# Performance work log

Hardware: AMD Instinct MI355X
Metric: run time of the kernel (lower is better)

## Reference

```python
import jax, jax.numpy as jnp
import numpy as np

N_PART = 22      # alanine dipeptide atoms
N_DIM = 3
H_IN = 8         # h_initial feature dim (before time concat)
HID = 64
N_LAYERS = 4
BATCH = 1024
E_LOCAL = N_PART * (N_PART - 1)  # fully connected, both directions


def _make_edges(batch):
    rows, cols = [], []
    for i in range(N_PART):
        for j in range(i + 1, N_PART):
            rows += [i, j]; cols += [j, i]
    rows = np.asarray(rows, np.int32); cols = np.asarray(cols, np.int32)
    offs = (np.arange(batch, dtype=np.int32) * N_PART)[:, None]
    return (jnp.asarray((rows[None, :] + offs).reshape(-1)),
            jnp.asarray((cols[None, :] + offs).reshape(-1)))


def setup_inputs() -> dict:
    key = jax.random.key(0)
    ks = jax.random.split(key, 16)
    g = lambda k, shape, s=0.1: jax.random.normal(k, shape, jnp.float32) * s
    rows, cols = _make_edges(BATCH)
    return {
        "t": jax.random.uniform(ks[0], (BATCH, 1), jnp.float32),
        "xs": jax.random.normal(ks[1], (BATCH, N_PART * N_DIM), jnp.float32),
        "h_initial": g(ks[2], (N_PART, H_IN), 1.0),
        "emb_w": g(ks[3], (H_IN + 1, HID)), "emb_b": jnp.zeros((HID,), jnp.float32),
        "edge_w1": g(ks[4], (N_LAYERS, 2 * HID + 2, HID)), "edge_b1": jnp.zeros((N_LAYERS, HID), jnp.float32),
        "edge_w2": g(ks[5], (N_LAYERS, HID, HID)), "edge_b2": jnp.zeros((N_LAYERS, HID), jnp.float32),
        "node_w1": g(ks[6], (N_LAYERS, 2 * HID, HID)), "node_b1": jnp.zeros((N_LAYERS, HID), jnp.float32),
        "node_w2": g(ks[7], (N_LAYERS, HID, HID)), "node_b2": jnp.zeros((N_LAYERS, HID), jnp.float32),
        "coord_w1": g(ks[8], (N_LAYERS, HID, HID)), "coord_b1": jnp.zeros((N_LAYERS, HID), jnp.float32),
        "coord_w2": g(ks[9], (N_LAYERS, HID, 1)),
        "rows": rows, "cols": cols,
    }


def reference(t, xs, h_initial, emb_w, emb_b,
              edge_w1, edge_b1, edge_w2, edge_b2,
              node_w1, node_b1, node_w2, node_b2,
              coord_w1, coord_b1, coord_w2, rows, cols):
    B = xs.shape[0]
    NN = B * N_PART
    x0 = xs.reshape(NN, N_DIM)
    # node features: tiled h_initial + time channel
    h = jnp.tile(h_initial[None], (B, 1, 1)).reshape(NN, H_IN)
    tt = jnp.tile(t, (1, N_PART)).reshape(NN, 1)
    h = jnp.concatenate([h, tt], axis=-1)                       # [NN, H_IN+1]
    # static edge attribute: initial squared distances
    edge_attr = jnp.sum((x0[rows] - x0[cols]) ** 2, axis=1, keepdims=True)  # [E,1]

    h = h @ emb_w + emb_b                                       # embedding (no act)
    x = x0
    for l in range(N_LAYERS):
        diff = x[rows] - x[cols]                                # [E,3]
        radial = jnp.sum(diff ** 2, axis=1, keepdims=True)      # [E,1]
        diff = diff / (jnp.sqrt(radial) + 1.0)                  # norm_diff=True
        # edge model
        e_in = jnp.concatenate([h[rows], h[cols], radial, edge_attr], axis=1)
        m = jax.nn.silu(e_in @ edge_w1[l] + edge_b1[l])
        m = jax.nn.silu(m @ edge_w2[l] + edge_b2[l])            # [E,HID]
        # coord model (coord_mlp last layer has no bias; coords_weight=1, agg='sum')
        phi_x = jax.nn.silu(m @ coord_w1[l] + coord_b1[l]) @ coord_w2[l]  # [E,1]
        x = x + jax.ops.segment_sum(diff * phi_x, rows, num_segments=NN)
        # node model (recurrent residual)
        agg = jax.ops.segment_sum(m, rows, num_segments=NN)     # [NN,HID]
        n_in = jnp.concatenate([h, agg], axis=1)
        h = h + (jax.nn.silu(n_in @ node_w1[l] + node_b1[l]) @ node_w2[l] + node_b2[l])

    vel = (x - x0).reshape(B, N_PART, N_DIM)
    vel = vel - jnp.mean(vel, axis=1, keepdims=True)            # remove_mean
    return vel.reshape(B, N_PART * N_DIM)
```

## Files before the change

### kernel.cpp

```cpp
#include <hip/hip_runtime.h>


#define NPART   22
#define NDIM    3
#define XDIM    (NPART * NDIM)
#define H_IN    8
#define HID     64
#define NLAYERS 4
#define EPB     (NPART * (NPART - 1))
#define BLOCK   256

__device__ __forceinline__ float silu_f(float x) {
    return __fdividef(x, 1.0f + __expf(-x));
}

#define ACC16(ARR, WPTR, E0) do {                                   \
    const float4* _w4 = (const float4*)(WPTR);                      \
    _Pragma("unroll")                                               \
    for (int _q = 0; _q < 16; ++_q) {                               \
        float4 _w = _w4[_q];                                        \
        ARR[4*_q+0] = fmaf((E0), _w.x, ARR[4*_q+0]);                \
        ARR[4*_q+1] = fmaf((E0), _w.y, ARR[4*_q+1]);                \
        ARR[4*_q+2] = fmaf((E0), _w.z, ARR[4*_q+2]);                \
        ARR[4*_q+3] = fmaf((E0), _w.w, ARR[4*_q+3]);                \
    }                                                               \
} while (0)

#define ACC8(ARR, WPTR, E0) do {                                    \
    const float4* _w4 = (const float4*)(WPTR);                      \
    float4 _wa = _w4[0], _wb = _w4[1];                              \
    ARR[0] = fmaf((E0), _wa.x, ARR[0]);                             \
    ARR[1] = fmaf((E0), _wa.y, ARR[1]);                             \
    ARR[2] = fmaf((E0), _wa.z, ARR[2]);                             \
    ARR[3] = fmaf((E0), _wa.w, ARR[3]);                             \
    ARR[4] = fmaf((E0), _wb.x, ARR[4]);                             \
    ARR[5] = fmaf((E0), _wb.y, ARR[5]);                             \
    ARR[6] = fmaf((E0), _wb.z, ARR[6]);                             \
    ARR[7] = fmaf((E0), _wb.w, ARR[7]);                             \
} while (0)

__global__ void __launch_bounds__(BLOCK)
w2_transpose_kernel(const float* __restrict__ w2, float* __restrict__ w2t) {
    int l = blockIdx.x;
    for (int i = threadIdx.x; i < HID * HID; i += BLOCK) {
        int k = i >> 6, j = i & 63;
        w2t[l * HID * HID + j * HID + k] = w2[l * HID * HID + k * HID + j];
    }
}

__device__ __forceinline__ void edge_rc(int e, int& r, int& c) {
    int k = e / NPART;
    r = e - k * NPART;
    c = r + 1 + k;
    if (c >= NPART) c -= NPART;
}

#define WC_RW   0
#define WC_EA   64
#define WC_EB2  128
#define WC_CB1  192
#define WC_CW2  256
#define WC_N    320

template <bool TRANSPOSED>
__global__ void __launch_bounds__(BLOCK)
egnn_fused_kernel(const float* __restrict__ t_in,
                  const float* __restrict__ xs,
                  const float* __restrict__ h_init,
                  const float* __restrict__ emb_w,
                  const float* __restrict__ emb_b,
                  const float* __restrict__ edge_w1,
                  const float* __restrict__ edge_b1,
                  const float* __restrict__ edge_w2x,
                  const float* __restrict__ edge_b2,
                  const float* __restrict__ node_w1,
                  const float* __restrict__ node_b1,
                  const float* __restrict__ node_w2,
                  const float* __restrict__ node_b2,
                  const float* __restrict__ coord_w1,
                  const float* __restrict__ coord_b1,
                  const float* __restrict__ coord_w2,
                  float*       __restrict__ out) {
    __shared__ float h_s   [HID * NPART];
    __shared__ float hagg_s[HID * NPART];
    __shared__ float ns_s  [HID * NPART];
    __shared__ float pr_s  [HID * NPART];
    __shared__ float pc_s  [HID * NPART];
    __shared__ float wc_s  [WC_N];
    __shared__ float x_s[XDIM], x0_s[XDIM], xacc_s[XDIM];
    __shared__ float ea_s[EPB];
    __shared__ float mean_s[NDIM];

    const int b   = blockIdx.x;
    const int tid = threadIdx.x;
    const float tval = t_in[b];

    if (tid < XDIM) {
        float v = xs[b * XDIM + tid];
        x0_s[tid] = v;
        x_s[tid]  = v;
    }
    for (int idx = tid; idx < NPART * HID; idx += BLOCK) {
        int n = idx >> 6, j = idx & 63;
        float acc = emb_b[j] + tval * emb_w[H_IN * HID + j];
#pragma unroll
        for (int k = 0; k < H_IN; ++k)
            acc = fmaf(h_init[n * H_IN + k], emb_w[k * HID + j], acc);
        h_s[j * NPART + n] = acc;
    }
    __syncthreads();
    for (int e = tid; e < EPB; e += BLOCK) {
        int r, c; edge_rc(e, r, c);
        float dx = x0_s[r*3+0] - x0_s[c*3+0];
        float dy = x0_s[r*3+1] - x0_s[c*3+1];
        float dz = x0_s[r*3+2] - x0_s[c*3+2];
        ea_s[e] = dx*dx + dy*dy + dz*dz;
    }
    __syncthreads();

#pragma unroll 1
    for (int l = 0; l < NLAYERS; ++l) {
        const float* ew1 = edge_w1  + l * (2*HID + 2) * HID;
        const float* eb1 = edge_b1  + l * HID;
        const float* w2x = edge_w2x + l * HID * HID;
        const float* eb2 = edge_b2  + l * HID;
        const float* cw1 = coord_w1 + l * HID * HID;
        const float* cb1 = coord_b1 + l * HID;
        const float* cw2 = coord_w2 + l * HID;
        const float* nw1 = node_w1  + l * 2 * HID * HID;
        const float* nb1 = node_b1  + l * HID;
        const float* nw2 = node_w2  + l * HID * HID;
        const float* nb2 = node_b2  + l * HID;

        for (int idx = tid; idx < NPART * HID; idx += BLOCK) hagg_s[idx] = 0.0f;
        if (tid < XDIM) xacc_s[tid] = 0.0f;
        for (int idx = tid; idx < WC_N; idx += BLOCK) {
            int g = idx >> 6, j = idx & 63;
            float v;
            if      (g == 0) v = ew1[(2 * HID) * HID + j];
            else if (g == 1) v = ew1[(2 * HID + 1) * HID + j];
            else if (g == 2) v = eb2[j];
            else if (g == 3) v = cb1[j];
            else             v = cw2[j];
            wc_s[idx] = v;
        }

        if (tid < NPART * 8) {
            int n = tid >> 3, jg = tid & 7;
            float pr[8], pc[8];
            {
                const float4* b4 = (const float4*)(eb1 + jg * 8);
                float4 wa = b4[0], wb = b4[1];
                pr[0]=wa.x; pr[1]=wa.y; pr[2]=wa.z; pr[3]=wa.w;
                pr[4]=wb.x; pr[5]=wb.y; pr[6]=wb.z; pr[7]=wb.w;
            }
#pragma unroll
            for (int jj = 0; jj < 8; ++jj) pc[jj] = 0.0f;
#pragma unroll 1
            for (int k = 0; k < HID; ++k) {
                float e0 = h_s[k * NPART + n];
                ACC8(pr, ew1 + k * HID + jg * 8, e0);
                ACC8(pc, ew1 + (HID + k) * HID + jg * 8, e0);
            }
#pragma unroll
            for (int jj = 0; jj < 8; ++jj) {
                pr_s[(jg * 8 + jj) * NPART + n] = pr[jj];
                pc_s[(jg * 8 + jj) * NPART + n] = pc[jj];
            }
        }
        __syncthreads();

#pragma unroll 1
        for (int e = tid; e < EPB; e += BLOCK) {
            int r, c; edge_rc(e, r, c);
            float dx = x_s[r*3+0] - x_s[c*3+0];
            float dy = x_s[r*3+1] - x_s[c*3+1];
            float dz = x_s[r*3+2] - x_s[c*3+2];
            float radial = dx*dx + dy*dy + dz*dz;
            float invn = __fdividef(1.0f, sqrtf(radial) + 1.0f);
            float ux = dx * invn, uy = dy * invn, uz = dz * invn;
            float ea = ea_s[e];

            float a[HID];
#pragma unroll
            for (int j = 0; j < HID; ++j) {
                float v = pr_s[j * NPART + r] + pc_s[j * NPART + c];
                v = fmaf(radial, wc_s[WC_RW + j], v);
                v = fmaf(ea,     wc_s[WC_EA + j], v);
                a[j] = silu_f(v);
            }

            float t1[HID];
#pragma unroll
            for (int q = 0; q < 16; ++q) {
                float4 w = ((const float4*)(wc_s + WC_CB1))[q];
                t1[4*q+0] = w.x; t1[4*q+1] = w.y;
                t1[4*q+2] = w.z; t1[4*q+3] = w.w;
            }

#pragma unroll 2
            for (int j = 0; j < HID; ++j) {
                float m0, m1, m2, m3;
                if constexpr (TRANSPOSED) {
                    const float4* w4 = (const float4*)(w2x + j * HID);
                    m0 = wc_s[WC_EB2 + j]; m1 = 0.0f; m2 = 0.0f; m3 = 0.0f;
#pragma unroll
                    for (int q = 0; q < 4; ++q) {
                        float4 wA = w4[4*q+0], wB = w4[4*q+1];
                        float4 wC = w4[4*q+2], wD = w4[4*q+3];
                        m0 = fmaf(a[16*q+ 0], wA.x, m0);
                        m0 = fmaf(a[16*q+ 1], wA.y, m0);
                        m0 = fmaf(a[16*q+ 2], wA.z, m0);
                        m0 = fmaf(a[16*q+ 3], wA.w, m0);
                        m1 = fmaf(a[16*q+ 4], wB.x, m1);
                        m1 = fmaf(a[16*q+ 5], wB.y, m1);
                        m1 = fmaf(a[16*q+ 6], wB.z, m1);
                        m1 = fmaf(a[16*q+ 7], wB.w, m1);
                        m2 = fmaf(a[16*q+ 8], wC.x, m2);
                        m2 = fmaf(a[16*q+ 9], wC.y, m2);
                        m2 = fmaf(a[16*q+10], wC.z, m2);
                        m2 = fmaf(a[16*q+11], wC.w, m2);
                        m3 = fmaf(a[16*q+12], wD.x, m3);
                        m3 = fmaf(a[16*q+13], wD.y, m3);
                        m3 = fmaf(a[16*q+14], wD.z, m3);
                        m3 = fmaf(a[16*q+15], wD.w, m3);
                    }
                } else {
                    m0 = wc_s[WC_EB2 + j]; m1 = 0.0f; m2 = 0.0f; m3 = 0.0f;
#pragma unroll
                    for (int k = 0; k < HID; k += 4) {
                        m0 = fmaf(a[k+0], w2x[(k+0) * HID + j], m0);
                        m1 = fmaf(a[k+1], w2x[(k+1) * HID + j], m1);
                        m2 = fmaf(a[k+2], w2x[(k+2) * HID + j], m2);
                        m3 = fmaf(a[k+3], w2x[(k+3) * HID + j], m3);
                    }
                }
                float mj = silu_f((m0 + m1) + (m2 + m3));
                atomicAdd(&hagg_s[j * NPART + r], mj);
                ACC16(t1, cw1 + j * HID, mj);
            }

            float phi = 0.0f;
#pragma unroll
            for (int q = 0; q < 16; ++q) {
                float4 w = ((const float4*)(wc_s + WC_CW2))[q];
                phi = fmaf(silu_f(t1[4*q+0]), w.x, phi);
                phi = fmaf(silu_f(t1[4*q+1]), w.y, phi);
                phi = fmaf(silu_f(t1[4*q+2]), w.z, phi);
                phi = fmaf(silu_f(t1[4*q+3]), w.w, phi);
            }
            atomicAdd(&xacc_s[r*3+0], ux * phi);
            atomicAdd(&xacc_s[r*3+1], uy * phi);
            atomicAdd(&xacc_s[r*3+2], uz * phi);
        }
        __syncthreads();

        if (tid < NPART * 8) {
            int n = tid >> 3, jg = tid & 7;
            float acc[8];
            {
                const float4* b4 = (const float4*)(nb1 + jg * 8);
                float4 wa = b4[0], wb = b4[1];
                acc[0]=wa.x; acc[1]=wa.y; acc[2]=wa.z; acc[3]=wa.w;
                acc[4]=wb.x; acc[5]=wb.y; acc[6]=wb.z; acc[7]=wb.w;
            }
#pragma unroll 1
            for (int k = 0; k < HID; ++k) {
                float e0 = h_s[k * NPART + n];
                ACC8(acc, nw1 + k * HID + jg * 8, e0);
            }
#pragma unroll 1
            for (int k = 0; k < HID; ++k) {
                float e0 = hagg_s[k * NPART + n];
                ACC8(acc, nw1 + (HID + k) * HID + jg * 8, e0);
            }
#pragma unroll
            for (int jj = 0; jj < 8; ++jj)
                ns_s[(jg * 8 + jj) * NPART + n] = silu_f(acc[jj]);
        }
        __syncthreads();
        if (tid < NPART * 8) {
            int n = tid >> 3, jg = tid & 7;
            float acc[8];
            {
                const float4* b4 = (const float4*)(nb2 + jg * 8);
                float4 wa = b4[0], wb = b4[1];
                acc[0]=wa.x; acc[1]=wa.y; acc[2]=wa.z; acc[3]=wa.w;
                acc[4]=wb.x; acc[5]=wb.y; acc[6]=wb.z; acc[7]=wb.w;
            }
#pragma unroll 1
            for (int k = 0; k < HID; ++k) {
                float e0 = ns_s[k * NPART + n];
                ACC8(acc, nw2 + k * HID + jg * 8, e0);
            }
#pragma unroll
            for (int jj = 0; jj < 8; ++jj)
                h_s[(jg * 8 + jj) * NPART + n] += acc[jj];
        } else if (tid >= NPART * 8 && tid < NPART * 8 + XDIM) {
            int i = tid - NPART * 8;
            x_s[i] += xacc_s[i];
        }
        __syncthreads();
    }

    if (tid < XDIM) xacc_s[tid] = x_s[tid] - x0_s[tid];
    __syncthreads();
    if (tid < NDIM) {
        float s = 0.0f;
#pragma unroll
        for (int n = 0; n < NPART; ++n) s += xacc_s[n * NDIM + tid];
        mean_s[tid] = s * (1.0f / NPART);
    }
    __syncthreads();
    if (tid < XDIM) {
        int d = tid - (tid / 3) * 3;
        out[b * XDIM + tid] = xacc_s[tid] - mean_s[d];
    }
}

extern "C" void kernel_launch(void* const* d_in, const int* in_sizes, int n_in,
                              void* d_out, int out_size, void* d_ws, size_t ws_size,
                              hipStream_t stream) {
    const float* t_in    = (const float*)d_in[0];
    const float* xs      = (const float*)d_in[1];
    const float* h_init  = (const float*)d_in[2];
    const float* emb_w   = (const float*)d_in[3];
    const float* emb_b   = (const float*)d_in[4];
    const float* edge_w1 = (const float*)d_in[5];
    const float* edge_b1 = (const float*)d_in[6];
    const float* edge_w2 = (const float*)d_in[7];
    const float* edge_b2 = (const float*)d_in[8];
    const float* node_w1 = (const float*)d_in[9];
    const float* node_b1 = (const float*)d_in[10];
    const float* node_w2 = (const float*)d_in[11];
    const float* node_b2 = (const float*)d_in[12];
    const float* coord_w1= (const float*)d_in[13];
    const float* coord_b1= (const float*)d_in[14];
    const float* coord_w2= (const float*)d_in[15];
    float* out = (float*)d_out;

    const int B = in_sizes[0];
    const size_t w2t_bytes = (size_t)NLAYERS * HID * HID * sizeof(float);

    if (ws_size >= w2t_bytes) {
        float* w2t = (float*)d_ws;
        hipLaunchKernelGGL(w2_transpose_kernel, dim3(NLAYERS), dim3(BLOCK), 0,
                           stream, edge_w2, w2t);
        hipLaunchKernelGGL((egnn_fused_kernel<true>), dim3(B), dim3(BLOCK), 0,
                           stream, t_in, xs, h_init, emb_w, emb_b,
                           edge_w1, edge_b1, w2t, edge_b2,
                           node_w1, node_b1, node_w2, node_b2,
                           coord_w1, coord_b1, coord_w2, out);
    } else {
        hipLaunchKernelGGL((egnn_fused_kernel<false>), dim3(B), dim3(BLOCK), 0,
                           stream, t_in, xs, h_init, emb_w, emb_b,
                           edge_w1, edge_b1, edge_w2, edge_b2,
                           node_w1, node_b1, node_w2, node_b2,
                           coord_w1, coord_b1, coord_w2, out);
    }
}
```

Measured before the change: 2.712 ms.

## Stage edge, coord and node MLP weights in shared memory per layer

Adds a 32 KB shared buffer that holds, for each layer, the edge second-layer weights (transposed when needed) and the coord first-layer weights during the edge phase, then node_w1 and node_w2 before their phases. The inner per-edge loops now read weights from LDS instead of global/L1, which removes repeated global loads from every thread. In exchange it adds LDS footprint, which may reduce blocks per CU, and extra syncthreads plus copy time per layer.

```diff
diff --git a/kernel.cpp b/kernel.cpp
--- a/kernel.cpp
+++ b/kernel.cpp
@@ -61,6 +61,8 @@
 #define WC_CB1  192
 #define WC_CW2  256
 #define WC_N    320
+
+#define WB_CW1  4096
 
 template <bool TRANSPOSED>
 __global__ void __launch_bounds__(BLOCK)
@@ -86,6 +88,7 @@
     __shared__ float ns_s  [HID * NPART];
     __shared__ float pr_s  [HID * NPART];
     __shared__ float pc_s  [HID * NPART];
+    __shared__ float wbuf_s[2 * HID * HID];
     __shared__ float wc_s  [WC_N];
     __shared__ float x_s[XDIM], x0_s[XDIM], xacc_s[XDIM];
     __shared__ float ea_s[EPB];
@@ -144,6 +147,17 @@
             else             v = cw2[j];
             wc_s[idx] = v;
         }
+        if constexpr (TRANSPOSED) {
+            for (int t = tid; t < 1024; t += BLOCK)
+                ((float4*)wbuf_s)[t] = ((const float4*)w2x)[t];
+        } else {
+            for (int idx = tid; idx < HID * HID; idx += BLOCK) {
+                int j = idx >> 6, k = idx & 63;
+                wbuf_s[idx] = w2x[k * HID + j];
+            }
+        }
+        for (int t = tid; t < 1024; t += BLOCK)
+            ((float4*)(wbuf_s + WB_CW1))[t] = ((const float4*)cw1)[t];
 
         if (tid < NPART * 8) {
             int n = tid >> 3, jg = tid & 7;
@@ -200,44 +214,32 @@
 
 #pragma unroll 2
             for (int j = 0; j < HID; ++j) {
-                float m0, m1, m2, m3;
-                if constexpr (TRANSPOSED) {
-                    const float4* w4 = (const float4*)(w2x + j * HID);
-                    m0 = wc_s[WC_EB2 + j]; m1 = 0.0f; m2 = 0.0f; m3 = 0.0f;
-#pragma unroll
-                    for (int q = 0; q < 4; ++q) {
-                        float4 wA = w4[4*q+0], wB = w4[4*q+1];
-                        float4 wC = w4[4*q+2], wD = w4[4*q+3];
-                        m0 = fmaf(a[16*q+ 0], wA.x, m0);
-                        m0 = fmaf(a[16*q+ 1], wA.y, m0);
-                        m0 = fmaf(a[16*q+ 2], wA.z, m0);
-                        m0 = fmaf(a[16*q+ 3], wA.w, m0);
-                        m1 = fmaf(a[16*q+ 4], wB.x, m1);
-                        m1 = fmaf(a[16*q+ 5], wB.y, m1);
-                        m1 = fmaf(a[16*q+ 6], wB.z, m1);
-                        m1 = fmaf(a[16*q+ 7], wB.w, m1);
-                        m2 = fmaf(a[16*q+ 8], wC.x, m2);
-                        m2 = fmaf(a[16*q+ 9], wC.y, m2);
-                        m2 = fmaf(a[16*q+10], wC.z, m2);
-                        m2 = fmaf(a[16*q+11], wC.w, m2);
-                        m3 = fmaf(a[16*q+12], wD.x, m3);
-                        m3 = fmaf(a[16*q+13], wD.y, m3);
-                        m3 = fmaf(a[16*q+14], wD.z, m3);
-                        m3 = fmaf(a[16*q+15], wD.w, m3);
-                    }
-                } else {
-                    m0 = wc_s[WC_EB2 + j]; m1 = 0.0f; m2 = 0.0f; m3 = 0.0f;
-#pragma unroll
-                    for (int k = 0; k < HID; k += 4) {
-                        m0 = fmaf(a[k+0], w2x[(k+0) * HID + j], m0);
-                        m1 = fmaf(a[k+1], w2x[(k+1) * HID + j], m1);
-                        m2 = fmaf(a[k+2], w2x[(k+2) * HID + j], m2);
-                        m3 = fmaf(a[k+3], w2x[(k+3) * HID + j], m3);
-                    }
+                const float4* w4 = (const float4*)(wbuf_s + j * HID);
+                float m0 = wc_s[WC_EB2 + j], m1 = 0.0f, m2 = 0.0f, m3 = 0.0f;
+#pragma unroll
+                for (int q = 0; q < 4; ++q) {
+                    float4 wA = w4[4*q+0], wB = w4[4*q+1];
+                    float4 wC = w4[4*q+2], wD = w4[4*q+3];
+                    m0 = fmaf(a[16*q+ 0], wA.x, m0);
+                    m0 = fmaf(a[16*q+ 1], wA.y, m0);
+                    m0 = fmaf(a[16*q+ 2], wA.z, m0);
+                    m0 = fmaf(a[16*q+ 3], wA.w, m0);
+                    m1 = fmaf(a[16*q+ 4], wB.x, m1);
+                    m1 = fmaf(a[16*q+ 5], wB.y, m1);
+                    m1 = fmaf(a[16*q+ 6], wB.z, m1);
+                    m1 = fmaf(a[16*q+ 7], wB.w, m1);
+                    m2 = fmaf(a[16*q+ 8], wC.x, m2);
+                    m2 = fmaf(a[16*q+ 9], wC.y, m2);
+                    m2 = fmaf(a[16*q+10], wC.z, m2);
+                    m2 = fmaf(a[16*q+11], wC.w, m2);
+                    m3 = fmaf(a[16*q+12], wD.x, m3);
+                    m3 = fmaf(a[16*q+13], wD.y, m3);
+                    m3 = fmaf(a[16*q+14], wD.z, m3);
+                    m3 = fmaf(a[16*q+15], wD.w, m3);
                 }
                 float mj = silu_f((m0 + m1) + (m2 + m3));
                 atomicAdd(&hagg_s[j * NPART + r], mj);
-                ACC16(t1, cw1 + j * HID, mj);
+                ACC16(t1, wbuf_s + WB_CW1 + j * HID, mj);
             }
 
             float phi = 0.0f;
@@ -253,6 +255,10 @@
             atomicAdd(&xacc_s[r*3+1], uy * phi);
             atomicAdd(&xacc_s[r*3+2], uz * phi);
         }
+        __syncthreads();
+
+        for (int t = tid; t < 2048; t += BLOCK)
+            ((float4*)wbuf_s)[t] = ((const float4*)nw1)[t];
         __syncthreads();
 
         if (tid < NPART * 8) {
@@ -267,18 +273,23 @@
 #pragma unroll 1
             for (int k = 0; k < HID; ++k) {
                 float e0 = h_s[k * NPART + n];
-                ACC8(acc, nw1 + k * HID + jg * 8, e0);
+                ACC8(acc, wbuf_s + k * HID + jg * 8, e0);
             }
 #pragma unroll 1
             for (int k = 0; k < HID; ++k) {
                 float e0 = hagg_s[k * NPART + n];
-                ACC8(acc, nw1 + (HID + k) * HID + jg * 8, e0);
+                ACC8(acc, wbuf_s + (HID + k) * HID + jg * 8, e0);
             }
 #pragma unroll
             for (int jj = 0; jj < 8; ++jj)
                 ns_s[(jg * 8 + jj) * NPART + n] = silu_f(acc[jj]);
         }
         __syncthreads();
+
+        for (int t = tid; t < 1024; t += BLOCK)
+            ((float4*)wbuf_s)[t] = ((const float4*)nw2)[t];
+        __syncthreads();
+
         if (tid < NPART * 8) {
             int n = tid >> 3, jg = tid & 7;
             float acc[8];
@@ -291,7 +302,7 @@
 #pragma unroll 1
             for (int k = 0; k < HID; ++k) {
                 float e0 = ns_s[k * NPART + n];
-                ACC8(acc, nw2 + k * HID + jg * 8, e0);
+                ACC8(acc, wbuf_s + k * HID + jg * 8, e0);
             }
 #pragma unroll
             for (int jj = 0; jj < 8; ++jj)
```

Result: slower. 2.951 ms (+8.8%).
